# Kernel tuning notes

Hardware: AMD Instinct MI355X
Metric: run time of the kernel (lower is better)

## Reference

```python
import jax, jax.numpy as jnp
import numpy as np

EMBED_DIM = 768
NUM_HEAD = 12
HEAD_DIM = EMBED_DIM // NUM_HEAD


def setup_inputs() -> dict:
    key = jax.random.key(0)
    ks = jax.random.split(key, 9)
    B, S, E = 1, 4096, EMBED_DIM
    s = 1.0 / np.sqrt(E)
    inp = {
        "x": jax.random.normal(ks[0], (B, S, E), dtype=jnp.float32),
        "mask": jnp.zeros((B, S), dtype=jnp.bool_),  # True = masked out (padding)
        "Wq": jax.random.normal(ks[1], (E, E), dtype=jnp.float32) * s,
        "bq": jnp.zeros((E,), dtype=jnp.float32),
        "Wk": jax.random.normal(ks[2], (E, E), dtype=jnp.float32) * s,
        "bk": jnp.zeros((E,), dtype=jnp.float32),
        "Wv": jax.random.normal(ks[3], (E, E), dtype=jnp.float32) * s,
        "bv": jnp.zeros((E,), dtype=jnp.float32),
        "Wo": jax.random.normal(ks[4], (E, E), dtype=jnp.float32) * s,
        "bo": jnp.zeros((E,), dtype=jnp.float32),
    }
    return inp


def reference(x, mask, Wq, bq, Wk, bk, Wv, bv, Wo, bo):
    B, S, E = x.shape
    H, D = NUM_HEAD, HEAD_DIM
    # QKV projections -> [B, H, S, D]
    q = (x @ Wq.T + bq).reshape(B, S, H, D).transpose(0, 2, 1, 3)
    k = (x @ Wk.T + bk).reshape(B, S, H, D).transpose(0, 2, 1, 3)
    v = (x @ Wv.T + bv).reshape(B, S, H, D).transpose(0, 2, 1, 3)
    # NOTE: original scales by sqrt(embed_dim), not sqrt(head_dim)
    attn = jnp.einsum("bhqd,bhkd->bhqk", q, k) / jnp.sqrt(jnp.float32(E))
    # mask: [B, S] -> broadcast over (head, query) dims; True -> -inf
    attn = jnp.where(mask[:, None, None, :], -jnp.inf, attn)
    attn = jax.nn.softmax(attn, axis=-1)  # same math as manual max-subtract softmax
    out = jnp.einsum("bhqk,bhkd->bhqd", attn, v)  # [B, H, S, D]
    out = out.transpose(0, 2, 1, 3).reshape(B, S, E)
    return out @ Wo.T + bo
```

## Files before the change

kernel.cpp:

```cpp
#include <hip/hip_runtime.h>
#include <hip/hip_bf16.h>
#include <math.h>

typedef __bf16 bf16;
typedef __attribute__((ext_vector_type(8))) __bf16 bf16x8;
typedef __attribute__((ext_vector_type(4))) __bf16 bf16x4;
typedef __attribute__((ext_vector_type(4))) float f32x4;
typedef __attribute__((ext_vector_type(16))) float f32x16;

typedef __attribute__((address_space(1))) void* as1ptr;
typedef __attribute__((address_space(3))) void* as3ptr;

__device__ __forceinline__ void gload16(const void* g, void* lds) {
  __builtin_amdgcn_global_load_lds((as1ptr)(unsigned long long)(g),
                                   (as3ptr)(unsigned long long)(lds), 16, 0, 0);
}

#define MFMA16(a, b, c) __builtin_amdgcn_mfma_f32_16x16x32_bf16((a), (b), (c), 0, 0, 0)
#define MFMA32(a, b, c) __builtin_amdgcn_mfma_f32_32x32x16_bf16((a), (b), (c), 0, 0, 0)
#define EXP2(x) __builtin_amdgcn_exp2f(x)
#define WAITV4 asm volatile("s_waitcnt vmcnt(4)" ::: "memory")
#define WAITV2 asm volatile("s_waitcnt vmcnt(2)" ::: "memory")
#define WAITV0 asm volatile("s_waitcnt vmcnt(0)" ::: "memory")
#define BAR() __builtin_amdgcn_s_barrier()
#define PRIO1() __builtin_amdgcn_s_setprio(1)
#define PRIO0() __builtin_amdgcn_s_setprio(0)

#define SEQ 4096
#define EMB 768
#define QSC (0.036084391824351615f * 1.4426950408889634f)

#define NCVT 2688
__global__ __launch_bounds__(256)
void cvt_all_kernel(const float* __restrict__ x, const float* __restrict__ Wq,
                    const float* __restrict__ Wk, const float* __restrict__ Wv,
                    const float* __restrict__ Wo,
                    bf16* __restrict__ xb, bf16* __restrict__ Wqb, bf16* __restrict__ Wkb,
                    bf16* __restrict__ Wvb, bf16* __restrict__ Wob,
                    const unsigned char* __restrict__ mask,
                    unsigned long long* __restrict__ tf64) {
  int b = blockIdx.x;
  if (b == NCVT) {
    int t = threadIdx.x;
    if (t < 64) {
      unsigned v = 0;
      const unsigned char* mp = mask + t * 64;
      for (int i = 0; i < 64; i++) v |= mp[i];
      unsigned long long bits = __ballot(v != 0);
      if (t == 0) *tf64 = bits;
    }
    return;
  }
  const float* in;
  bf16* out;
  int base;
  if (b < 1536) {
    in = x; out = xb; base = b;
  } else {
    int r = b - 1536, seg = r / 288, off = r % 288;
    in  = (seg == 0) ? Wq  : (seg == 1) ? Wk  : (seg == 2) ? Wv  : Wo;
    out = (seg == 0) ? Wqb : (seg == 1) ? Wkb : (seg == 2) ? Wvb : Wob;
    base = off;
  }
  int i = (base * 256 + threadIdx.x) * 8;
  float4 a = *(const float4*)(in + i);
  float4 c = *(const float4*)(in + i + 4);
  bf16x8 v;
  v[0] = (bf16)a.x; v[1] = (bf16)a.y; v[2] = (bf16)a.z; v[3] = (bf16)a.w;
  v[4] = (bf16)c.x; v[5] = (bf16)c.y; v[6] = (bf16)c.z; v[7] = (bf16)c.w;
  *(bf16x8*)(out + i) = v;
}

__global__ __launch_bounds__(256)
void gemm_qkv_kernel(const bf16* __restrict__ A,
                     const bf16* __restrict__ B0, const bf16* __restrict__ B1,
                     const bf16* __restrict__ B2,
                     const float* __restrict__ bias0, const float* __restrict__ bias1,
                     const float* __restrict__ bias2,
                     bf16* __restrict__ Qh, char* __restrict__ Kswz,
                     char* __restrict__ Vswz) {
  __shared__ __attribute__((aligned(16))) char Asb[3][8192];
  __shared__ __attribute__((aligned(16))) char Bsb[3][8192];
  const int tid = threadIdx.x;
  const int wid = tid >> 6, lane = tid & 63;
  const int g = lane >> 4, c16 = lane & 15;
  const int wr = wid >> 1, wc = wid & 1;
  const int bm0 = blockIdx.x * 128;

  const int mat = blockIdx.y / 6;
  const int nb = (blockIdx.y % 6) * 128;
  const bf16* Bp = (mat == 0) ? B0 : (mat == 1 ? B1 : B2);
  const float* bias = (mat == 0) ? bias0 : (mat == 1 ? bias1 : bias2);

  const int arow = tid >> 2, acol = (tid & 3) * 16;

#define STAGE_G(k, b)                                                              \
  do {                                                                             \
    gload16((const char*)A + (size_t)(bm0 + arow) * (EMB * 2) + (k)*64 + acol,     \
            &Asb[b][wid * 1024]);                                                  \
    gload16((const char*)A + (size_t)(bm0 + 64 + arow) * (EMB * 2) + (k)*64 + acol,\
            &Asb[b][4096 + wid * 1024]);                                           \
    gload16((const char*)Bp + (size_t)(nb + arow) * (EMB * 2) + (k)*64 + acol,     \
            &Bsb[b][wid * 1024]);                                                  \
    gload16((const char*)Bp + (size_t)(nb + 64 + arow) * (EMB * 2) + (k)*64 + acol,\
            &Bsb[b][4096 + wid * 1024]);                                           \
  } while (0)

  f32x4 acc[4][4];
#pragma unroll
  for (int i = 0; i < 4; i++)
#pragma unroll
    for (int j = 0; j < 4; j++) acc[i][j] = f32x4{0.f, 0.f, 0.f, 0.f};

#define COMPUTE_G(cur)                                                         \
  do {                                                                         \
    bf16x8 a[4], b[4];                                                         \
    _Pragma("unroll") for (int i = 0; i < 4; i++)                              \
        a[i] = *(const bf16x8*)(&Asb[cur][(wr * 64 + i * 16 + c16) * 64 + g * 16]); \
    _Pragma("unroll") for (int j = 0; j < 4; j++)                              \
        b[j] = *(const bf16x8*)(&Bsb[cur][(wc * 64 + j * 16 + c16) * 64 + g * 16]); \
    PRIO1();                                                                   \
    _Pragma("unroll") for (int i = 0; i < 4; i++)                              \
        _Pragma("unroll") for (int j = 0; j < 4; j++)                          \
            acc[i][j] = MFMA16(a[i], b[j], acc[i][j]);                         \
    PRIO0();                                                                   \
  } while (0)

  STAGE_G(0, 0);
  STAGE_G(1, 1);
  int cur = 0;
  for (int kk = 0; kk < EMB / 32 - 1; ++kk) {
    WAITV4;
    BAR();
    if (kk < EMB / 32 - 2) {
      int stb = (cur == 0) ? 2 : cur - 1;
      STAGE_G(kk + 2, stb);
    }
    COMPUTE_G(cur);
    cur = (cur == 2) ? 0 : cur + 1;
  }
  WAITV0;
  BAR();
  COMPUTE_G(cur);
#undef STAGE_G
#undef COMPUTE_G

#pragma unroll
  for (int i = 0; i < 4; i++) {
#pragma unroll
    for (int j = 0; j < 4; j++) {
      int colL = nb + wc * 64 + j * 16 + c16;
      float bval = bias[colL];
#pragma unroll
      for (int r = 0; r < 4; r++) {
        int row = bm0 + wr * 64 + i * 16 + 4 * g + r;
        float val = acc[i][j][r] + bval;
        int hh = colL >> 6, d = colL & 63;
        if (mat == 0) {
          Qh[((size_t)hh * SEQ + row) * 64 + d] = (bf16)(val * QSC);
        } else if (mat == 1) {
          *(bf16*)(Kswz + ((size_t)hh * SEQ + row) * 128 +
                   ((d * 2) ^ ((row & 7) << 4))) = (bf16)val;
        } else {
          int kk2 = row & 63;
          int cc = (kk2 & 48) | (kk2 & 3) | ((kk2 & 4) << 1) | ((kk2 & 8) >> 1);
          *(bf16*)(Vswz + ((size_t)hh * 64 + d) * 8192 + (size_t)(row >> 6) * 128 +
                   ((cc * 2) ^ ((d & 7) << 4))) = (bf16)val;
        }
      }
    }
  }
}

__global__ __launch_bounds__(256)
void gemm_out_kernel(const bf16* __restrict__ A, const bf16* __restrict__ B,
                     const float* __restrict__ bias, float* __restrict__ outF) {
  __shared__ __attribute__((aligned(16))) char Asb[3][4096];
  __shared__ __attribute__((aligned(16))) char Bsb[3][4096];
  const int tid = threadIdx.x;
  const int wid = tid >> 6, lane = tid & 63;
  const int g = lane >> 4, c16 = lane & 15;
  const int wr = wid >> 1, wc = wid & 1;
  const int bm0 = blockIdx.x * 64, nb = blockIdx.y * 64;
  const int arow = tid >> 2, acol = (tid & 3) * 16;

#define STAGE_O(k, b)                                                          \
  do {                                                                         \
    gload16((const char*)A + (size_t)(bm0 + arow) * (EMB * 2) + (k)*64 + acol, \
            &Asb[b][wid * 1024]);                                              \
    gload16((const char*)B + (size_t)(nb + arow) * (EMB * 2) + (k)*64 + acol,  \
            &Bsb[b][wid * 1024]);                                              \
  } while (0)

  f32x4 acc[2][2];
#pragma unroll
  for (int i = 0; i < 2; i++)
#pragma unroll
    for (int j = 0; j < 2; j++) acc[i][j] = f32x4{0.f, 0.f, 0.f, 0.f};

#define COMPUTE_O(cur)                                                         \
  do {                                                                         \
    bf16x8 a[2], b[2];                                                         \
    _Pragma("unroll") for (int i = 0; i < 2; i++)                              \
        a[i] = *(const bf16x8*)(&Asb[cur][(wr * 32 + i * 16 + c16) * 64 + g * 16]); \
    _Pragma("unroll") for (int j = 0; j < 2; j++)                              \
        b[j] = *(const bf16x8*)(&Bsb[cur][(wc * 32 + j * 16 + c16) * 64 + g * 16]); \
    PRIO1();                                                                   \
    _Pragma("unroll") for (int i = 0; i < 2; i++)                              \
        _Pragma("unroll") for (int j = 0; j < 2; j++)                          \
            acc[i][j] = MFMA16(a[i], b[j], acc[i][j]);                         \
    PRIO0();                                                                   \
  } while (0)

  STAGE_O(0, 0);
  STAGE_O(1, 1);
  int cur = 0;
  for (int kk = 0; kk < EMB / 32 - 1; ++kk) {
    WAITV2;
    BAR();
    if (kk < EMB / 32 - 2) {
      int stb = (cur == 0) ? 2 : cur - 1;
      STAGE_O(kk + 2, stb);
    }
    COMPUTE_O(cur);
    cur = (cur == 2) ? 0 : cur + 1;
  }
  WAITV0;
  BAR();
  COMPUTE_O(cur);
#undef STAGE_O
#undef COMPUTE_O

#pragma unroll
  for (int i = 0; i < 2; i++) {
#pragma unroll
    for (int j = 0; j < 2; j++) {
      int colL = nb + wc * 32 + j * 16 + c16;
      float bval = bias[colL];
#pragma unroll
      for (int r = 0; r < 4; r++) {
        int row = bm0 + wr * 32 + i * 16 + 4 * g + r;
        outF[(size_t)row * EMB + colL] = acc[i][j][r] + bval;
      }
    }
  }
}

__global__ __launch_bounds__(512)
void attn_kernel(const char* __restrict__ Kswz, const char* __restrict__ Vswz,
                 const bf16* __restrict__ Qh, const unsigned char* __restrict__ mask,
                 const unsigned long long* __restrict__ tf64,
                 bf16* __restrict__ P0, bf16* __restrict__ P1, float* __restrict__ lm) {
  __shared__ __attribute__((aligned(16))) char LBUF[49152];
  char* LK = LBUF;
  char* LV = LBUF + 24576;
  const int tid = threadIdx.x;
  const int wid = tid >> 6, lane = tid & 63;
  const int qh = wid >> 1, kh = wid & 1;
  const int l31 = lane & 31, hi = lane >> 5;
  const int bsw = ((blockIdx.x & 7) * 96) + (blockIdx.x >> 3);
  const int h = bsw >> 6;
  const int rem = bsw & 63;
  const int qb = rem >> 1;
  const int ks = rem & 1;
  const unsigned long long tfb = *tf64;
  const int NT = 32;

  bf16x8 qa[4];
  {
    const bf16* qp = Qh + ((size_t)h * SEQ + qb * 128 + qh * 32 + l31) * 64 + hi * 8;
    qa[0] = *(const bf16x8*)(qp);
    qa[1] = *(const bf16x8*)(qp + 16);
    qa[2] = *(const bf16x8*)(qp + 32);
    qa[3] = *(const bf16x8*)(qp + 48);
  }
  bf16x8 onesA;
#pragma unroll
  for (int e = 0; e < 8; ++e) onesA[e] = (bf16)1.0f;

  f32x16 ot0, ot1, lacc;
#pragma unroll
  for (int r = 0; r < 16; r++) { ot0[r] = 0.f; ot1[r] = 0.f; lacc[r] = 0.f; }

  const char* ksrc = Kswz + (size_t)h * SEQ * 128 + (size_t)ks * 2048 * 128 + tid * 16;
  const char* vsrc = Vswz + ((size_t)h * 64 + (tid >> 3)) * 8192 + ks * 4096 + (tid & 7) * 16;

#define STAGE(t, b)                                              \
  do {                                                           \
    gload16(ksrc + (size_t)(t)*8192, LK + (b)*8192 + wid * 1024);\
    gload16(vsrc + (size_t)(t)*128,  LV + (b)*8192 + wid * 1024);\
  } while (0)

  const int krow = kh * 32 + l31;
  const int ksw = (krow & 7) << 4;
  const int vsw = (l31 & 7) << 4;
  const int vcb = kh * 64 + hi * 16;

#define COMPUTE(t, cur)                                                          \
  do {                                                                           \
    const char* Kb = LK + (cur)*8192;                                            \
    const char* Vb = LV + (cur)*8192;                                            \
    bf16x8 kf0 = *(const bf16x8*)(Kb + krow * 128 + ((hi * 16) ^ ksw));          \
    bf16x8 kf1 = *(const bf16x8*)(Kb + krow * 128 + ((32 + hi * 16) ^ ksw));     \
    bf16x8 kf2 = *(const bf16x8*)(Kb + krow * 128 + ((64 + hi * 16) ^ ksw));     \
    bf16x8 kf3 = *(const bf16x8*)(Kb + krow * 128 + ((96 + hi * 16) ^ ksw));     \
    f32x16 s;                                                                    \
    _Pragma("unroll") for (int r = 0; r < 16; r++) s[r] = 0.f;                   \
    PRIO1();                                                                     \
    s = MFMA32(kf0, qa[0], s);                                                   \
    s = MFMA32(kf1, qa[1], s);                                                   \
    s = MFMA32(kf2, qa[2], s);                                                   \
    s = MFMA32(kf3, qa[3], s);                                                   \
    PRIO0();                                                                     \
    if (tfb & (1ull << (ks * 32 + (t)))) {                                       \
      _Pragma("unroll") for (int r = 0; r < 16; r++) {                           \
        int key = ks * 2048 + (t)*64 + kh * 32 + (r & 3) + 8 * (r >> 2) + 4 * hi;\
        if (mask[key]) s[r] = -INFINITY;                                         \
      }                                                                          \
    }                                                                            \
    float p[16];                                                                 \
    _Pragma("unroll") for (int r = 0; r < 16; r++) p[r] = EXP2(s[r]);            \
    bf16x8 pb0, pb1;                                                             \
    _Pragma("unroll") for (int e = 0; e < 8; ++e) {                              \
      pb0[e] = (bf16)p[e];                                                       \
      pb1[e] = (bf16)p[8 + e];                                                   \
    }                                                                            \
    bf16x8 vf00 = *(const bf16x8*)(Vb + l31 * 128 + ((vcb) ^ vsw));              \
    bf16x8 vf01 = *(const bf16x8*)(Vb + l31 * 128 + ((vcb + 32) ^ vsw));         \
    bf16x8 vf10 = *(const bf16x8*)(Vb + (32 + l31) * 128 + ((vcb) ^ vsw));       \
    bf16x8 vf11 = *(const bf16x8*)(Vb + (32 + l31) * 128 + ((vcb + 32) ^ vsw));  \
    PRIO1();                                                                     \
    ot0 = MFMA32(vf00, pb0, ot0);                                                \
    ot0 = MFMA32(vf01, pb1, ot0);                                                \
    ot1 = MFMA32(vf10, pb0, ot1);                                                \
    ot1 = MFMA32(vf11, pb1, ot1);                                                \
    lacc = MFMA32(onesA, pb0, lacc);                                             \
    lacc = MFMA32(onesA, pb1, lacc);                                             \
    PRIO0();                                                                     \
  } while (0)

  STAGE(0, 0);
  STAGE(1, 1);
  int cur = 0;
  for (int t = 0; t < NT - 1; ++t) {
    WAITV2;
    BAR();
    if (t < NT - 2) {
      int stb = (cur == 0) ? 2 : cur - 1;
      STAGE(t + 2, stb);
    }
    COMPUTE(t, cur);
    cur = (cur == 2) ? 0 : cur + 1;
  }
  WAITV0;
  BAR();
  COMPUTE(NT - 1, cur);
#undef STAGE
#undef COMPUTE

  float l_ = lacc[0];

  __syncthreads();
  float* ml = (float*)(LBUF + 32768);
  ml[wid * 64 + lane] = l_;
  __syncthreads();
  const int pw = wid ^ 1;
  float lt = l_ + ml[pw * 64 + lane];
  char* obase = LBUF + qh * 8192 + lane * 128;
  const int osw = (lane & 7) << 4;
  if (kh == 1) {
#pragma unroll
    for (int u = 0; u < 4; ++u) {
      *(f32x4*)(obase + ((u * 16) ^ osw)) =
          f32x4{ot0[4 * u], ot0[4 * u + 1], ot0[4 * u + 2], ot0[4 * u + 3]};
      *(f32x4*)(obase + (((4 + u) * 16) ^ osw)) =
          f32x4{ot1[4 * u], ot1[4 * u + 1], ot1[4 * u + 2], ot1[4 * u + 3]};
    }
  }
  __syncthreads();
  if (kh == 0) {
    float inv = 1.f / lt;
    int tok = qb * 128 + qh * 32 + l31;
    bf16* Op = ks ? P1 : P0;
    bf16* op = Op + (size_t)tok * EMB + h * 64;
#pragma unroll
    for (int u = 0; u < 4; ++u) {
      f32x4 w0 = *(const f32x4*)(obase + ((u * 16) ^ osw));
      f32x4 w1 = *(const f32x4*)(obase + (((4 + u) * 16) ^ osw));
      bf16x4 o0, o1;
#pragma unroll
      for (int e = 0; e < 4; ++e) {
        o0[e] = (bf16)((ot0[4 * u + e] + w0[e]) * inv);
        o1[e] = (bf16)((ot1[4 * u + e] + w1[e]) * inv);
      }
      *(bf16x4*)(op + 8 * u + 4 * hi) = o0;
      *(bf16x4*)(op + 32 + 8 * u + 4 * hi) = o1;
    }
    if (lane < 32) {
      lm[(((size_t)ks * 12 + h) * 4096 + tok) * 2 + 1] = lt;
    }
  }
}

__global__ __launch_bounds__(256)
void merge_kernel(bf16* __restrict__ P0, const bf16* __restrict__ P1,
                  const float* __restrict__ lm) {
  int idx = (blockIdx.x * 256 + threadIdx.x) * 8;
  int tok = idx / EMB;
  int e0 = idx % EMB;
  int h = e0 >> 6;
  float l0 = lm[((size_t)h * 4096 + tok) * 2 + 1];
  float l1 = lm[(((size_t)12 + h) * 4096 + tok) * 2 + 1];
  float inv = 1.f / (l0 + l1);
  float w0 = l0 * inv;
  float w1 = l1 * inv;
  bf16x8 a = *(const bf16x8*)(P0 + idx);
  bf16x8 b = *(const bf16x8*)(P1 + idx);
  bf16x8 o;
#pragma unroll
  for (int e = 0; e < 8; ++e) o[e] = (bf16)(w0 * (float)a[e] + w1 * (float)b[e]);
  *(bf16x8*)(P0 + idx) = o;
}

extern "C" void kernel_launch(void* const* d_in, const int* in_sizes, int n_in,
                              void* d_out, int out_size, void* d_ws, size_t ws_size,
                              hipStream_t stream) {
  (void)in_sizes; (void)n_in; (void)out_size; (void)ws_size;
  const float* x = (const float*)d_in[0];
  const unsigned char* mask = (const unsigned char*)d_in[1];
  const float* Wq = (const float*)d_in[2];
  const float* bq = (const float*)d_in[3];
  const float* Wk = (const float*)d_in[4];
  const float* bk = (const float*)d_in[5];
  const float* Wv = (const float*)d_in[6];
  const float* bv = (const float*)d_in[7];
  const float* Wo = (const float*)d_in[8];
  const float* bo = (const float*)d_in[9];
  float* out = (float*)d_out;
  char* ws = (char*)d_ws;

  bf16* xb   = (bf16*)(ws + 0);
  bf16* Wqb  = (bf16*)(ws + 6291456);
  bf16* Wkb  = (bf16*)(ws + 7471104);
  bf16* Wvb  = (bf16*)(ws + 8650752);
  bf16* Wob  = (bf16*)(ws + 9830400);
  bf16* Qh   = (bf16*)(ws + 11010048);
  char* Kswz = ws + 17301504;
  char* Vswz = ws + 23592960;
  bf16* Obuf = (bf16*)(ws + 29884416);
  unsigned long long* tf64 = (unsigned long long*)(ws + 36175872);
  float* lmArr = (float*)(ws + 36179968);
  bf16* P1 = xb;

  cvt_all_kernel<<<NCVT + 1, 256, 0, stream>>>(x, Wq, Wk, Wv, Wo, xb, Wqb, Wkb, Wvb,
                                               Wob, mask, tf64);
  gemm_qkv_kernel<<<dim3(32, 18), 256, 0, stream>>>(
      xb, Wqb, Wkb, Wvb, bq, bk, bv, Qh, Kswz, Vswz);
  attn_kernel<<<768, 512, 0, stream>>>(Kswz, Vswz, Qh, mask, tf64, Obuf, P1, lmArr);
  merge_kernel<<<1536, 256, 0, stream>>>(Obuf, P1, lmArr);
  gemm_out_kernel<<<dim3(64, 12), 256, 0, stream>>>(Obuf, Wob, bo, out);
}
```

Baseline: 123.2 us.

## Fuse split-KV merge into output GEMM A-load and halve QKV GEMM M-tile

Removes the separate merge kernel. The output projection GEMM now loads both partial attention outputs plus their softmax sums, blends them in registers and writes the result to LDS as its A operand, using a two-stage buffer with a full wait each iteration. Separately, the QKV GEMM tile drops from 128 to 64 rows, doubling its grid to improve CU occupancy and balance. The trade-off is one fewer launch and no round trip of the merged buffer through memory, against a shallower, more synchronous pipeline in the output GEMM, and each Wo tile now redoing the blend for every column block.

```diff
diff --git a/kernel.cpp b/kernel.cpp
--- a/kernel.cpp
+++ b/kernel.cpp
@@ -19,9 +19,10 @@
 #define MFMA16(a, b, c) __builtin_amdgcn_mfma_f32_16x16x32_bf16((a), (b), (c), 0, 0, 0)
 #define MFMA32(a, b, c) __builtin_amdgcn_mfma_f32_32x32x16_bf16((a), (b), (c), 0, 0, 0)
 #define EXP2(x) __builtin_amdgcn_exp2f(x)
-#define WAITV4 asm volatile("s_waitcnt vmcnt(4)" ::: "memory")
+#define WAITV3 asm volatile("s_waitcnt vmcnt(3)" ::: "memory")
 #define WAITV2 asm volatile("s_waitcnt vmcnt(2)" ::: "memory")
 #define WAITV0 asm volatile("s_waitcnt vmcnt(0)" ::: "memory")
+#define WAITLG0 asm volatile("s_waitcnt lgkmcnt(0)" ::: "memory")
 #define BAR() __builtin_amdgcn_s_barrier()
 #define PRIO1() __builtin_amdgcn_s_setprio(1)
 #define PRIO0() __builtin_amdgcn_s_setprio(0)
@@ -79,13 +80,13 @@
                      const float* __restrict__ bias2,
                      bf16* __restrict__ Qh, char* __restrict__ Kswz,
                      char* __restrict__ Vswz) {
-  __shared__ __attribute__((aligned(16))) char Asb[3][8192];
+  __shared__ __attribute__((aligned(16))) char Asb[3][4096];
   __shared__ __attribute__((aligned(16))) char Bsb[3][8192];
   const int tid = threadIdx.x;
   const int wid = tid >> 6, lane = tid & 63;
   const int g = lane >> 4, c16 = lane & 15;
   const int wr = wid >> 1, wc = wid & 1;
-  const int bm0 = blockIdx.x * 128;
+  const int bm0 = blockIdx.x * 64;
 
   const int mat = blockIdx.y / 6;
   const int nb = (blockIdx.y % 6) * 128;
@@ -98,29 +99,27 @@
   do {                                                                             \
     gload16((const char*)A + (size_t)(bm0 + arow) * (EMB * 2) + (k)*64 + acol,     \
             &Asb[b][wid * 1024]);                                                  \
-    gload16((const char*)A + (size_t)(bm0 + 64 + arow) * (EMB * 2) + (k)*64 + acol,\
-            &Asb[b][4096 + wid * 1024]);                                           \
     gload16((const char*)Bp + (size_t)(nb + arow) * (EMB * 2) + (k)*64 + acol,     \
             &Bsb[b][wid * 1024]);                                                  \
     gload16((const char*)Bp + (size_t)(nb + 64 + arow) * (EMB * 2) + (k)*64 + acol,\
             &Bsb[b][4096 + wid * 1024]);                                           \
   } while (0)
 
-  f32x4 acc[4][4];
-#pragma unroll
-  for (int i = 0; i < 4; i++)
+  f32x4 acc[2][4];
+#pragma unroll
+  for (int i = 0; i < 2; i++)
 #pragma unroll
     for (int j = 0; j < 4; j++) acc[i][j] = f32x4{0.f, 0.f, 0.f, 0.f};
 
 #define COMPUTE_G(cur)                                                         \
   do {                                                                         \
-    bf16x8 a[4], b[4];                                                         \
-    _Pragma("unroll") for (int i = 0; i < 4; i++)                              \
-        a[i] = *(const bf16x8*)(&Asb[cur][(wr * 64 + i * 16 + c16) * 64 + g * 16]); \
+    bf16x8 a[2], b[4];                                                         \
+    _Pragma("unroll") for (int i = 0; i < 2; i++)                              \
+        a[i] = *(const bf16x8*)(&Asb[cur][(wr * 32 + i * 16 + c16) * 64 + g * 16]); \
     _Pragma("unroll") for (int j = 0; j < 4; j++)                              \
         b[j] = *(const bf16x8*)(&Bsb[cur][(wc * 64 + j * 16 + c16) * 64 + g * 16]); \
     PRIO1();                                                                   \
-    _Pragma("unroll") for (int i = 0; i < 4; i++)                              \
+    _Pragma("unroll") for (int i = 0; i < 2; i++)                              \
         _Pragma("unroll") for (int j = 0; j < 4; j++)                          \
             acc[i][j] = MFMA16(a[i], b[j], acc[i][j]);                         \
     PRIO0();                                                                   \
@@ -130,7 +129,7 @@
   STAGE_G(1, 1);
   int cur = 0;
   for (int kk = 0; kk < EMB / 32 - 1; ++kk) {
-    WAITV4;
+    WAITV3;
     BAR();
     if (kk < EMB / 32 - 2) {
       int stb = (cur == 0) ? 2 : cur - 1;
@@ -146,14 +145,14 @@
 #undef COMPUTE_G
 
 #pragma unroll
-  for (int i = 0; i < 4; i++) {
+  for (int i = 0; i < 2; i++) {
 #pragma unroll
     for (int j = 0; j < 4; j++) {
       int colL = nb + wc * 64 + j * 16 + c16;
       float bval = bias[colL];
 #pragma unroll
       for (int r = 0; r < 4; r++) {
-        int row = bm0 + wr * 64 + i * 16 + 4 * g + r;
+        int row = bm0 + wr * 32 + i * 16 + 4 * g + r;
         float val = acc[i][j][r] + bval;
         int hh = colL >> 6, d = colL & 63;
         if (mat == 0) {
@@ -173,24 +172,42 @@
 }
 
 __global__ __launch_bounds__(256)
-void gemm_out_kernel(const bf16* __restrict__ A, const bf16* __restrict__ B,
+void gemm_out_kernel(const bf16* __restrict__ P0, const bf16* __restrict__ P1,
+                     const float* __restrict__ lm, const bf16* __restrict__ B,
                      const float* __restrict__ bias, float* __restrict__ outF) {
-  __shared__ __attribute__((aligned(16))) char Asb[3][4096];
-  __shared__ __attribute__((aligned(16))) char Bsb[3][4096];
+  __shared__ __attribute__((aligned(16))) char Asb[2][4096];
+  __shared__ __attribute__((aligned(16))) char Bsb[2][4096];
   const int tid = threadIdx.x;
   const int wid = tid >> 6, lane = tid & 63;
   const int g = lane >> 4, c16 = lane & 15;
   const int wr = wid >> 1, wc = wid & 1;
   const int bm0 = blockIdx.x * 64, nb = blockIdx.y * 64;
   const int arow = tid >> 2, acol = (tid & 3) * 16;
-
-#define STAGE_O(k, b)                                                          \
-  do {                                                                         \
-    gload16((const char*)A + (size_t)(bm0 + arow) * (EMB * 2) + (k)*64 + acol, \
-            &Asb[b][wid * 1024]);                                              \
-    gload16((const char*)B + (size_t)(nb + arow) * (EMB * 2) + (k)*64 + acol,  \
-            &Bsb[b][wid * 1024]);                                              \
-  } while (0)
+  const int tok = bm0 + arow;
+
+#define ALOAD(kk, va, vb, vl0, vl1)                                \
+  do {                                                             \
+    int k0 = (kk)*32 + (tid & 3) * 8;                              \
+    int hd = k0 >> 6;                                              \
+    va = *(const bf16x8*)(P0 + (size_t)tok * EMB + k0);            \
+    vb = *(const bf16x8*)(P1 + (size_t)tok * EMB + k0);            \
+    vl0 = lm[((size_t)hd * 4096 + tok) * 2 + 1];                   \
+    vl1 = lm[(((size_t)12 + hd) * 4096 + tok) * 2 + 1];            \
+  } while (0)
+
+#define ABLEND(b, va, vb, vl0, vl1)                                \
+  do {                                                             \
+    float inv = 1.f / (vl0 + vl1);                                 \
+    float w0 = vl0 * inv, w1 = vl1 * inv;                          \
+    bf16x8 v;                                                      \
+    _Pragma("unroll") for (int e = 0; e < 8; ++e)                  \
+        v[e] = (bf16)(w0 * (float)va[e] + w1 * (float)vb[e]);      \
+    *(bf16x8*)(&Asb[b][tid * 16]) = v;                             \
+  } while (0)
+
+#define BSTAGE(kk, b)                                                          \
+  gload16((const char*)B + (size_t)(nb + arow) * (EMB * 2) + (kk)*64 + acol,   \
+          &Bsb[b][wid * 1024])
 
   f32x4 acc[2][2];
 #pragma unroll
@@ -212,23 +229,31 @@
     PRIO0();                                                                   \
   } while (0)
 
-  STAGE_O(0, 0);
-  STAGE_O(1, 1);
-  int cur = 0;
-  for (int kk = 0; kk < EMB / 32 - 1; ++kk) {
-    WAITV2;
+  const int NK = EMB / 32;
+  {
+    bf16x8 a0, a1;
+    float l0, l1;
+    ALOAD(0, a0, a1, l0, l1);
+    BSTAGE(0, 0);
+    ABLEND(0, a0, a1, l0, l1);
+  }
+  for (int kk = 0; kk < NK; ++kk) {
+    WAITV0;
+    WAITLG0;
     BAR();
-    if (kk < EMB / 32 - 2) {
-      int stb = (cur == 0) ? 2 : cur - 1;
-      STAGE_O(kk + 2, stb);
-    }
-    COMPUTE_O(cur);
-    cur = (cur == 2) ? 0 : cur + 1;
-  }
-  WAITV0;
-  BAR();
-  COMPUTE_O(cur);
-#undef STAGE_O
+    bf16x8 a0, a1;
+    float l0, l1;
+    const int nxt = kk + 1;
+    if (nxt < NK) {
+      ALOAD(nxt, a0, a1, l0, l1);
+      BSTAGE(nxt, nxt & 1);
+    }
+    COMPUTE_O(kk & 1);
+    if (nxt < NK) ABLEND(nxt & 1, a0, a1, l0, l1);
+  }
+#undef ALOAD
+#undef ABLEND
+#undef BSTAGE
 #undef COMPUTE_O
 
 #pragma unroll
@@ -402,26 +427,6 @@
   }
 }
 
-__global__ __launch_bounds__(256)
-void merge_kernel(bf16* __restrict__ P0, const bf16* __restrict__ P1,
-                  const float* __restrict__ lm) {
-  int idx = (blockIdx.x * 256 + threadIdx.x) * 8;
-  int tok = idx / EMB;
-  int e0 = idx % EMB;
-  int h = e0 >> 6;
-  float l0 = lm[((size_t)h * 4096 + tok) * 2 + 1];
-  float l1 = lm[(((size_t)12 + h) * 4096 + tok) * 2 + 1];
-  float inv = 1.f / (l0 + l1);
-  float w0 = l0 * inv;
-  float w1 = l1 * inv;
-  bf16x8 a = *(const bf16x8*)(P0 + idx);
-  bf16x8 b = *(const bf16x8*)(P1 + idx);
-  bf16x8 o;
-#pragma unroll
-  for (int e = 0; e < 8; ++e) o[e] = (bf16)(w0 * (float)a[e] + w1 * (float)b[e]);
-  *(bf16x8*)(P0 + idx) = o;
-}
-
 extern "C" void kernel_launch(void* const* d_in, const int* in_sizes, int n_in,
                               void* d_out, int out_size, void* d_ws, size_t ws_size,
                               hipStream_t stream) {
@@ -454,9 +459,8 @@
 
   cvt_all_kernel<<<NCVT + 1, 256, 0, stream>>>(x, Wq, Wk, Wv, Wo, xb, Wqb, Wkb, Wvb,
                                                Wob, mask, tf64);
-  gemm_qkv_kernel<<<dim3(32, 18), 256, 0, stream>>>(
+  gemm_qkv_kernel<<<dim3(64, 18), 256, 0, stream>>>(
       xb, Wqb, Wkb, Wvb, bq, bk, bv, Qh, Kswz, Vswz);
   attn_kernel<<<768, 512, 0, stream>>>(Kswz, Vswz, Qh, mask, tf64, Obuf, P1, lmArr);
-  merge_kernel<<<1536, 256, 0, stream>>>(Obuf, P1, lmArr);
-  gemm_out_kernel<<<dim3(64, 12), 256, 0, stream>>>(Obuf, Wob, bo, out);
-}
+  gemm_out_kernel<<<dim3(64, 12), 256, 0, stream>>>(Obuf, P1, lmArr, Wob, bo, out);
+}
```

New measurement: 128.9 us. +4.6%, slower.
